# Kernel tuning notes

Measured on AMD Instinct MI355X. Metric: run time of the kernel, lower is better.

The kernel has to match this reference:

```python
import math
import jax, jax.numpy as jnp
import numpy as np

B, SX, SY, D, H = 2, 1024, 1024, 1024, 16
FULL = 1536   # padded (full_q == full_k) frame length for the two-source attention
N_CTX = 2048  # causal bias buffer size
HD = D // H
LENS_X = np.array([1024, 700])
LENS_Y = np.array([1024, 850])


def _heads(t):
    b, s, d = t.shape
    return t.reshape(b, s, H, HD).transpose(0, 2, 1, 3)  # [B,H,S,HD]


def _merge(t):
    b, h, s, hd = t.shape
    return t.transpose(0, 2, 1, 3).reshape(b, s, h * hd)


def setup_inputs() -> dict:
    key = jax.random.key(0)
    ks = jax.random.split(key, 8)
    s = 0.02
    # ragged pack/unpack index lists: take = positions in the FULL frame, fill = positions in the shrunk frame
    x_take_b = np.concatenate([np.full(l, b, np.int32) for b, l in enumerate(LENS_X)])
    x_take_p = np.concatenate([(FULL - l + np.arange(l)).astype(np.int32) for l in LENS_X])  # right-aligned
    x_fill_b = x_take_b.copy()
    x_fill_p = np.concatenate([np.arange(l, dtype=np.int32) for l in LENS_X])
    y_take_b = np.concatenate([np.full(l, b, np.int32) for b, l in enumerate(LENS_Y)])
    y_take_p = np.concatenate([np.arange(l, dtype=np.int32) for l in LENS_Y])  # left-aligned
    y_fill_b = y_take_b.copy()
    y_fill_p = y_take_p.copy()
    # additive padding mask for the self-attention over shrunk x
    mask = np.full((B, 1, 1, SX), -10000.0, np.float32)
    for b, l in enumerate(LENS_X):
        mask[b, :, :, :l] = 0.0
    return {
        "x": jax.random.normal(ks[0], (B, SX, D), jnp.float32),
        "y": jax.random.normal(ks[1], (B, SY, D), jnp.float32),
        "attention_mask_x": jnp.asarray(mask),
        "W_attn": jax.random.normal(ks[2], (D, 3 * D), jnp.float32) * s,
        "b_attn": jnp.zeros((3 * D,), jnp.float32),
        "W_2a": jax.random.normal(ks[3], (D, D), jnp.float32) * s,
        "b_2a": jnp.zeros((D,), jnp.float32),
        "W_2b": jax.random.normal(ks[4], (D, 2 * D), jnp.float32) * s,
        "b_2b": jnp.zeros((2 * D,), jnp.float32),
        "W_proj": jax.random.normal(ks[5], (2 * D, D), jnp.float32) * s,
        "b_proj": jnp.zeros((D,), jnp.float32),
        "x_take_b": jnp.asarray(x_take_b), "x_take_p": jnp.asarray(x_take_p),
        "x_fill_b": jnp.asarray(x_fill_b), "x_fill_p": jnp.asarray(x_fill_p),
        "y_take_b": jnp.asarray(y_take_b), "y_take_p": jnp.asarray(y_take_p),
        "y_fill_b": jnp.asarray(y_fill_b), "y_fill_p": jnp.asarray(y_fill_p),
    }


def reference(x, y, attention_mask_x, W_attn, b_attn, W_2a, b_2a, W_2b, b_2b,
              W_proj, b_proj, x_take_b, x_take_p, x_fill_b, x_fill_p,
              y_take_b, y_take_p, y_fill_b, y_fill_p):
    causal = jnp.tril(jnp.ones((N_CTX, N_CTX), jnp.float32))
    inv_sqrt = 1.0 / math.sqrt(HD)

    # --- branch 1: causal self-attention on shrunk x ---
    qkv = x @ W_attn + b_attn
    q, k, v = jnp.split(qkv, 3, axis=2)
    q, k, v = _heads(q), _heads(k), _heads(v)
    w = jnp.einsum('bhqd,bhkd->bhqk', q, k) * inv_sqrt  # [B,H,SX,SX]
    b1 = causal[:SX, :SX]
    w = w * b1 - 10000.0 * (1.0 - b1) + attention_mask_x
    a = jnp.einsum('bhqk,bhkd->bhqd', jax.nn.softmax(w, axis=-1), v)
    a = _merge(a)  # [B,SX,D]

    # --- branch 2: two-source attention with ragged expand/shrink ---
    q2 = _heads(x @ W_2a + b_2a)                      # [B,H,SX,HD]
    k2, v2 = jnp.split(y @ W_2b + b_2b, 2, axis=2)
    k2, v2 = _heads(k2), _heads(v2)                   # [B,H,SY,HD]
    w2 = jnp.einsum('bhqd,bhkd->bhqk', q2, k2)        # [B,H,SX,SY] (unscaled yet)
    # expand key dim: shrunk SY -> FULL
    temp = jnp.zeros((B, H, SX, FULL), w2.dtype)
    temp = temp.at[y_take_b, :, :, y_take_p].set(w2[y_fill_b, :, :, y_fill_p])
    # expand query dim: shrunk SX -> FULL
    new_w = jnp.zeros((B, H, FULL, FULL), w2.dtype)
    new_w = new_w.at[x_take_b, :, x_take_p, :].set(temp[x_fill_b, :, x_fill_p, :])
    new_v = jnp.zeros((B, H, FULL, HD), v2.dtype)
    new_v = new_v.at[y_take_b, :, y_take_p, :].set(v2[y_fill_b, :, y_fill_p, :])
    kmask = jnp.full((B, 1, 1, FULL), -10000.0, w2.dtype)
    kmask = kmask.at[y_take_b, :, :, y_take_p].set(0.0)
    new_w = new_w * inv_sqrt
    b2 = causal[:FULL, :FULL]  # ns-nd == 0 since full_q == full_k
    new_w = new_w * b2 - 10000.0 * (1.0 - b2) + kmask
    a2 = jnp.einsum('bhqk,bhkd->bhqd', jax.nn.softmax(new_w, axis=-1), new_v)  # [B,H,FULL,HD]
    # shrink query dim back: FULL -> SX
    a2s = jnp.zeros((B, H, SX, HD), a2.dtype)
    a2s = a2s.at[x_fill_b, :, x_fill_p, :].set(a2[x_take_b, :, x_take_p, :])
    a2m = _merge(a2s)  # [B,SX,D]

    out = jnp.concatenate([a, a2m], axis=2) @ W_proj + b_proj  # [B,SX,D]
    return out
```

## Files before the change

kernel.cpp:

```cpp
#include <hip/hip_runtime.h>
#include <hip/hip_bf16.h>

typedef __bf16 bf16;
typedef __attribute__((ext_vector_type(4))) __bf16 bf16x4;
typedef __attribute__((ext_vector_type(8))) __bf16 bf16x8;
typedef __attribute__((ext_vector_type(4))) float floatx4;

__device__ __forceinline__ void gl_lds16(const bf16* g, bf16* l) {
  __builtin_amdgcn_global_load_lds(
      (const __attribute__((address_space(1))) void*)g,
      (__attribute__((address_space(3))) void*)l, 16, 0, 0);
}

__global__ __launch_bounds__(256) void sentinel_kernel(float* out, int n, float code) {
  int i = blockIdx.x * 256 + threadIdx.x;
  if (i < n) out[i] = code;
}

struct TP { const float* W; bf16* WT; int K; int N; int bxn; int bid0; };

__global__ __launch_bounds__(256) void prep_kernel(TP t0, TP t1, TP t2, TP t3,
                                                   const float* __restrict__ x,
                                                   const float* __restrict__ y,
                                                   bf16* __restrict__ xb,
                                                   bf16* __restrict__ yb) {
  int bid = blockIdx.x;
  int tid = threadIdx.x;
  if (bid < 2048) {
    __shared__ float tile[64][65];
    TP t = t0;
    if (bid >= t3.bid0) t = t3;
    else if (bid >= t2.bid0) t = t2;
    else if (bid >= t1.bid0) t = t1;
    int rb = bid - t.bid0;
    int n0 = (rb % t.bxn) * 64, k0 = (rb / t.bxn) * 64;
    int tx = tid & 15, ty = tid >> 4;
#pragma unroll
    for (int i = 0; i < 4; ++i) {
      floatx4 v = *(const floatx4*)(t.W + (size_t)(k0 + ty + 16 * i) * t.N + n0 + tx * 4);
#pragma unroll
      for (int j = 0; j < 4; ++j) tile[ty + 16 * i][tx * 4 + j] = v[j];
    }
    __syncthreads();
#pragma unroll
    for (int i = 0; i < 4; ++i) {
      int nr = ty + 16 * i;
      bf16x4 o;
#pragma unroll
      for (int j = 0; j < 4; ++j) o[j] = (bf16)tile[tx * 4 + j][nr];
      *(bf16x4*)(t.WT + (size_t)(n0 + nr) * t.K + k0 + tx * 4) = o;
    }
  } else {
    long base = (long)(bid - 2048) * 4096 + (long)tid * 16;
    const float* src = x; bf16* dst = xb; long idx = base;
    if (base >= 2097152) { src = y; dst = yb; idx = base - 2097152; }
    floatx4 v0 = *(const floatx4*)(src + idx);
    floatx4 v1 = *(const floatx4*)(src + idx + 4);
    floatx4 v2 = *(const floatx4*)(src + idx + 8);
    floatx4 v3 = *(const floatx4*)(src + idx + 12);
    bf16x8 o0, o1;
#pragma unroll
    for (int i = 0; i < 4; ++i) {
      o0[i] = (bf16)v0[i]; o0[4 + i] = (bf16)v1[i];
      o1[i] = (bf16)v2[i]; o1[4 + i] = (bf16)v3[i];
    }
    *(bf16x8*)(dst + idx) = o0;
    *(bf16x8*)(dst + idx + 8) = o1;
  }
}

struct GP { const bf16* A; const bf16* WT; const float* bias; bf16* C; bf16* VT;
            int N; int ldc; int vcol0; int bxn; int bid0; };

__global__ __launch_bounds__(256) void proj3_kernel(GP g0, GP g1, GP g2) {
  __shared__ __attribute__((aligned(16))) bf16 As[128 * 64];
  __shared__ __attribute__((aligned(16))) bf16 Bs[128 * 64];
  int bid = blockIdx.x;
  GP g = g0;
  if (bid >= g2.bid0) g = g2;
  else if (bid >= g1.bid0) g = g1;
  int rb = bid - g.bid0;
  int row0 = (rb / g.bxn) * 128, col0 = (rb % g.bxn) * 128;
  const int K = 1024;
  int tid = threadIdx.x;
  int lane = tid & 63, wave = tid >> 6;
  int quad = lane >> 4, l16 = lane & 15;
  int wm = wave >> 1, wn = wave & 1;
  floatx4 acc[4][4] = {};
  for (int k0 = 0; k0 < K; k0 += 64) {
#pragma unroll
    for (int s = 0; s < 4; ++s) {
      int sl = s * 256 + tid;
      int r = sl >> 3, o = sl & 7;
      int c = (o ^ (r & 7)) * 8;
      gl_lds16(g.WT + (size_t)(col0 + r) * K + k0 + c, Bs + (size_t)sl * 8);
      gl_lds16(g.A + (size_t)(row0 + r) * K + k0 + c, As + (size_t)sl * 8);
    }
    __syncthreads();
#pragma unroll
    for (int kk = 0; kk < 2; ++kk) {
      int ko = kk * 4 + quad;
      bf16x8 afr[4], bfr[4];
#pragma unroll
      for (int r = 0; r < 4; ++r) {
        int m = wm * 64 + r * 16 + l16;
        afr[r] = *(const bf16x8*)(As + (size_t)(m * 8 + (ko ^ (m & 7))) * 8);
      }
#pragma unroll
      for (int c = 0; c < 4; ++c) {
        int n = wn * 64 + c * 16 + l16;
        bfr[c] = *(const bf16x8*)(Bs + (size_t)(n * 8 + (ko ^ (n & 7))) * 8);
      }
#pragma unroll
      for (int r = 0; r < 4; ++r)
#pragma unroll
        for (int c = 0; c < 4; ++c)
          acc[r][c] = __builtin_amdgcn_mfma_f32_16x16x32_bf16(afr[r], bfr[c], acc[r][c], 0, 0, 0);
    }
    __syncthreads();
  }
  int inV = (col0 >= g.vcol0);
#pragma unroll
  for (int c = 0; c < 4; ++c) {
    int gcol = col0 + wn * 64 + c * 16 + l16;
    float bv = g.bias[gcol];
    if (inV) {
      int vcol = gcol - g.vcol0;
      int hh = vcol >> 6, dd = vcol & 63;
#pragma unroll
      for (int r = 0; r < 4; ++r) {
        int row = row0 + wm * 64 + r * 16 + quad * 4;
        int bb = row >> 10, key = row & 1023;
        bf16x4 pk;
#pragma unroll
        for (int e = 0; e < 4; ++e) pk[e] = (bf16)(acc[r][c][e] + bv);
        *(bf16x4*)(g.VT + ((size_t)((bb << 4) + hh)) * 65536 + (size_t)dd * 1024 + key) = pk;
      }
    } else {
#pragma unroll
      for (int r = 0; r < 4; ++r) {
        int grow = row0 + wm * 64 + r * 16 + quad * 4;
#pragma unroll
        for (int e = 0; e < 4; ++e)
          g.C[(size_t)(grow + e) * g.ldc + gcol] = (bf16)(acc[r][c][e] + bv);
      }
    }
  }
}

__global__ __launch_bounds__(256) void gemm_out_kernel(const bf16* __restrict__ A,
                                                       const bf16* __restrict__ WT,
                                                       const float* __restrict__ bias,
                                                       float* __restrict__ C,
                                                       int N, int K) {
  __shared__ __attribute__((aligned(16))) bf16 As[64 * 64];
  __shared__ __attribute__((aligned(16))) bf16 Bs[64 * 64];
  int tid = threadIdx.x;
  int lane = tid & 63, wave = tid >> 6;
  int quad = lane >> 4, l16 = lane & 15;
  int row0 = blockIdx.y * 64, col0 = blockIdx.x * 64;
  floatx4 acc[4] = {};
  for (int k0 = 0; k0 < K; k0 += 64) {
#pragma unroll
    for (int s = 0; s < 2; ++s) {
      int sl = s * 256 + tid;
      int r = sl >> 3, o = sl & 7;
      int c = (o ^ (r & 7)) * 8;
      gl_lds16(A + (size_t)(row0 + r) * K + k0 + c, As + (size_t)sl * 8);
      gl_lds16(WT + (size_t)(col0 + r) * K + k0 + c, Bs + (size_t)sl * 8);
    }
    __syncthreads();
#pragma unroll
    for (int kk = 0; kk < 2; ++kk) {
      int ko = kk * 4 + quad;
      int m = wave * 16 + l16;
      bf16x8 af = *(const bf16x8*)(As + (size_t)(m * 8 + (ko ^ (m & 7))) * 8);
#pragma unroll
      for (int nt = 0; nt < 4; ++nt) {
        int n = nt * 16 + l16;
        bf16x8 bf = *(const bf16x8*)(Bs + (size_t)(n * 8 + (ko ^ (n & 7))) * 8);
        acc[nt] = __builtin_amdgcn_mfma_f32_16x16x32_bf16(af, bf, acc[nt], 0, 0, 0);
      }
    }
    __syncthreads();
  }
#pragma unroll
  for (int nt = 0; nt < 4; ++nt) {
    int gcol = col0 + nt * 16 + l16;
    float bv = bias[gcol];
#pragma unroll
    for (int e = 0; e < 4; ++e) {
      int grow = row0 + wave * 16 + quad * 4 + e;
      C[(size_t)grow * N + gcol] = acc[nt][e] + bv;
    }
  }
}

struct AP {
  const bf16* Q; const bf16* K; const bf16* VT; bf16* O;
  int qstride, kstride, ostride;
  long qbatch, kbatch, obatch;
  int coff0, coff1, klen0, klen1, qv0, qv1;
};

__global__ __launch_bounds__(512) void attn2x_kernel(AP a0, AP a1, float scale) {
  __shared__ __attribute__((aligned(16))) bf16 Ks[2][64 * 64];
  __shared__ __attribute__((aligned(16))) bf16 Vs[2][64 * 64];
  __shared__ __attribute__((aligned(16))) bf16 Ps[8][16 * 72];
  AP a = (blockIdx.x >> 8) ? a1 : a0;
  int tid = threadIdx.x;
  int lane = tid & 63, w = tid >> 6;
  int quad = lane >> 4, l16 = lane & 15;
  int r = blockIdx.x & 255;
  int b = r >> 7, h = (r >> 3) & 15, qt = r & 7;
  int coff = b ? a.coff1 : a.coff0;
  int klen = b ? a.klen1 : a.klen0;
  int qv = b ? a.qv1 : a.qv0;
  int qbase = qt * 128;
  int wq0 = qbase + w * 16;
  int qi = wq0 + l16;
  const bf16* Q   = a.Q + (size_t)b * a.qbatch + h * 64;
  const bf16* Kp  = a.K + (size_t)b * a.kbatch + h * 64;
  const bf16* VTp = a.VT + (size_t)(b * 16 + h) * 65536;
  bf16* O = a.O + (size_t)b * a.obatch + h * 64;

  bf16x8 aq0 = *(const bf16x8*)(Q + (size_t)qi * a.qstride + quad * 8);
  bf16x8 aq1 = *(const bf16x8*)(Q + (size_t)qi * a.qstride + 32 + quad * 8);

  floatx4 o[4] = {};
  float part = 0.f;

  int kend = klen < qbase + 128 + coff ? klen : qbase + 128 + coff;
  int nblk = (kend + 63) >> 6;
  int wkend0 = wq0 + 16 + coff;
  int wkend = klen < wkend0 ? klen : wkend0;

  const float KSC = scale * 1.44269504f;
  const float KOFF = -5.77078016f;

  auto stage = [&](int buf, int j0) {
    int row = tid >> 3, ch = tid & 7;
    gl_lds16(Kp + (size_t)(j0 + row) * a.kstride + ((ch ^ (row & 7)) * 8),
             Ks[buf] + (size_t)tid * 8);
    gl_lds16(VTp + (size_t)row * 1024 + j0 + ((ch ^ (row & 7)) * 8),
             Vs[buf] + (size_t)tid * 8);
  };

  stage(0, 0);
  for (int t = 0; t < nblk; ++t) {
    int j0 = t * 64;
    __syncthreads();
    if (t + 1 < nblk) stage((t + 1) & 1, j0 + 64);
    if (j0 >= wkend) continue;
    const bf16* Kt = Ks[t & 1];
    const bf16* Vt = Vs[t & 1];

    floatx4 sv[4];
#pragma unroll
    for (int nt = 0; nt < 4; ++nt) {
      int key = nt * 16 + l16;
      int sl0 = key * 8 + (quad ^ (key & 7));
      int sl1 = key * 8 + ((quad + 4) ^ (key & 7));
      bf16x8 bk0 = *(const bf16x8*)(Kt + (size_t)sl0 * 8);
      bf16x8 bk1 = *(const bf16x8*)(Kt + (size_t)sl1 * 8);
      floatx4 z = {};
      z = __builtin_amdgcn_mfma_f32_16x16x32_bf16(bk0, aq0, z, 0, 0, 0);
      z = __builtin_amdgcn_mfma_f32_16x16x32_bf16(bk1, aq1, z, 0, 0, 0);
      sv[nt] = z;
    }
    bool fullv = (j0 + 63 <= wq0 + coff) && (j0 + 63 < klen);
#pragma unroll
    for (int nt = 0; nt < 4; ++nt) {
      bf16x4 pk;
#pragma unroll
      for (int e = 0; e < 4; ++e) {
        float arg = fmaf(sv[nt][e], KSC, KOFF);
        if (!fullv) {
          int j = j0 + nt * 16 + quad * 4 + e;
          arg = (j <= qi + coff && j < klen) ? arg : -60.0f;
        }
        float p = exp2f(arg);
        part += p;
        pk[e] = (bf16)p;
      }
      *(bf16x4*)(Ps[w] + l16 * 72 + nt * 16 + quad * 4) = pk;
    }
    bf16x8 pb0 = *(const bf16x8*)(Ps[w] + l16 * 72 + quad * 8);
    bf16x8 pb1 = *(const bf16x8*)(Ps[w] + l16 * 72 + 32 + quad * 8);
#pragma unroll
    for (int ct = 0; ct < 4; ++ct) {
      int dd = ct * 16 + l16;
      int sl0 = dd * 8 + (quad ^ (dd & 7));
      int sl1 = dd * 8 + ((quad + 4) ^ (dd & 7));
      bf16x8 va0 = *(const bf16x8*)(Vt + (size_t)sl0 * 8);
      bf16x8 va1 = *(const bf16x8*)(Vt + (size_t)sl1 * 8);
      o[ct] = __builtin_amdgcn_mfma_f32_16x16x32_bf16(va0, pb0, o[ct], 0, 0, 0);
      o[ct] = __builtin_amdgcn_mfma_f32_16x16x32_bf16(va1, pb1, o[ct], 0, 0, 0);
    }
  }
  part += __shfl_xor(part, 16);
  part += __shfl_xor(part, 32);
  float rinv = 1.0f / part;
#pragma unroll
  for (int ct = 0; ct < 4; ++ct) {
    bf16x4 pk;
#pragma unroll
    for (int e = 0; e < 4; ++e) {
      float val = o[ct][e] * rinv;
      if (qi >= qv) val = 0.f;
      pk[e] = (bf16)val;
    }
    *(bf16x4*)(O + (size_t)qi * a.ostride + ct * 16 + quad * 4) = pk;
  }
}

extern "C" void kernel_launch(void* const* d_in, const int* in_sizes, int n_in,
                              void* d_out, int out_size, void* d_ws, size_t ws_size,
                              hipStream_t stream) {
  const float* x      = (const float*)d_in[0];
  const float* y      = (const float*)d_in[1];
  const float* W_attn = (const float*)d_in[3];
  const float* b_attn = (const float*)d_in[4];
  const float* W_2a   = (const float*)d_in[5];
  const float* b_2a   = (const float*)d_in[6];
  const float* W_2b   = (const float*)d_in[7];
  const float* b_2b   = (const float*)d_in[8];
  const float* W_proj = (const float*)d_in[9];
  const float* b_proj = (const float*)d_in[10];
  bf16* ws = (bf16*)d_ws;
  float* out = (float*)d_out;

  const int LX0 = 1024, LX1 = 700, LY0 = 1024, LY1 = 850;
  const float scale = 0.125f;
  const size_t WS_FAST = (size_t)25165824 * 2;

  if (ws_size < WS_FAST) {
    sentinel_kernel<<<(out_size + 255) / 256, 256, 0, stream>>>(
        out, out_size, (float)(ws_size >> 20) + 10.0f);
    return;
  }

  bf16* qk1  = ws;
  bf16* q2   = ws + (size_t) 4194304;
  bf16* k2   = ws + (size_t) 6291456;
  bf16* VT1  = ws + (size_t) 8388608;
  bf16* VT2  = ws + (size_t)10485760;
  bf16* xb   = ws + (size_t)12582912;
  bf16* yb   = ws + (size_t)14680064;
  bf16* cat  = ws + (size_t)12582912;
  bf16* WaT  = ws + (size_t)16777216;
  bf16* W2aT = ws + (size_t)19922944;
  bf16* W2bT = ws + (size_t)20971520;
  bf16* WpT  = ws + (size_t)23068672;

  TP t0 = {W_attn, WaT, 1024, 3072, 48, 0};
  TP t1 = {W_2a, W2aT, 1024, 1024, 16, 768};
  TP t2 = {W_2b, W2bT, 1024, 2048, 32, 1024};
  TP t3 = {W_proj, WpT, 2048, 1024, 16, 1536};
  prep_kernel<<<3072, 256, 0, stream>>>(t0, t1, t2, t3, x, y, xb, yb);

  GP g0 = {xb, WaT, b_attn, qk1, VT1, 3072, 2048, 2048, 24, 0};
  GP g1 = {xb, W2aT, b_2a, q2, nullptr, 1024, 1024, 1 << 30, 8, 384};
  GP g2 = {yb, W2bT, b_2b, k2, VT2, 2048, 1024, 1024, 16, 512};
  proj3_kernel<<<768, 256, 0, stream>>>(g0, g1, g2);

  AP a0 = {qk1, qk1 + 1024, VT1, cat, 2048, 2048, 2048,
           (long)1024 * 2048, (long)1024 * 2048, (long)1024 * 2048,
           0, 0, LX0, LX1, 1024, 1024};
  AP a1 = {q2, k2, VT2, cat + 1024, 1024, 1024, 2048,
           (long)1024 * 1024, (long)1024 * 1024, (long)1024 * 2048,
           1536 - LX0, 1536 - LX1, LY0, LY1, LX0, LX1};
  attn2x_kernel<<<512, 512, 0, stream>>>(a0, a1, scale);

  gemm_out_kernel<<<dim3(16, 32), 256, 0, stream>>>(cat, WpT, b_proj, out, 1024, 2048);
}
```

Measured before the change: 233.8 us.

## Rework projection GEMM as 256x256 tile double-buffered ping-pong pipeline

Moves the fused QKV/q2/kv2 projection GEMM to 256x256 output tiles with 512 threads per block. LDS is double-buffered and each K-step is split into four phases, so global-to-LDS loads for the next tiles overlap the current MFMA work, with barriers and s_setprio steering the wave schedule. The goal is more operand reuse and hiding load latency instead of a full sync per K-step. The trade-off is that the grid shrinks from 768 to 192 blocks, fewer than the CU count, and the 128 KB LDS per block limits occupancy.

```diff
diff --git a/kernel.cpp b/kernel.cpp
--- a/kernel.cpp
+++ b/kernel.cpp
@@ -72,53 +72,161 @@
 struct GP { const bf16* A; const bf16* WT; const float* bias; bf16* C; bf16* VT;
             int N; int ldc; int vcol0; int bxn; int bid0; };
 
-__global__ __launch_bounds__(256) void proj3_kernel(GP g0, GP g1, GP g2) {
-  __shared__ __attribute__((aligned(16))) bf16 As[128 * 64];
-  __shared__ __attribute__((aligned(16))) bf16 Bs[128 * 64];
+__global__ __launch_bounds__(512, 2) void proj3_kernel(GP g0, GP g1, GP g2) {
+  __shared__ __attribute__((aligned(16))) bf16 As[2][16384];
+  __shared__ __attribute__((aligned(16))) bf16 Bs[2][16384];
   int bid = blockIdx.x;
   GP g = g0;
   if (bid >= g2.bid0) g = g2;
   else if (bid >= g1.bid0) g = g1;
   int rb = bid - g.bid0;
-  int row0 = (rb / g.bxn) * 128, col0 = (rb % g.bxn) * 128;
-  const int K = 1024;
+  int row0 = (rb / g.bxn) * 256, col0 = (rb % g.bxn) * 256;
   int tid = threadIdx.x;
   int lane = tid & 63, wave = tid >> 6;
   int quad = lane >> 4, l16 = lane & 15;
-  int wm = wave >> 1, wn = wave & 1;
-  floatx4 acc[4][4] = {};
-  for (int k0 = 0; k0 < K; k0 += 64) {
-#pragma unroll
-    for (int s = 0; s < 4; ++s) {
-      int sl = s * 256 + tid;
-      int r = sl >> 3, o = sl & 7;
-      int c = (o ^ (r & 7)) * 8;
-      gl_lds16(g.WT + (size_t)(col0 + r) * K + k0 + c, Bs + (size_t)sl * 8);
-      gl_lds16(g.A + (size_t)(row0 + r) * K + k0 + c, As + (size_t)sl * 8);
-    }
-    __syncthreads();
+  int wm = wave >> 2, wn = wave & 3;
+  const bf16* Ag = g.A + (size_t)row0 * 1024;
+  const bf16* Bg = g.WT + (size_t)col0 * 1024;
+
+  auto stA = [&](bf16* L, int k0, int qr) {
+#pragma unroll
+    for (int t = 0; t < 2; ++t) {
+      int i = t * 512 + tid;
+      int rh = i >> 3, o = i & 7;
+      int m = qr * 64 + (rh & 63) + ((rh & 64) << 1);
+      gl_lds16(Ag + (size_t)m * 1024 + k0 + ((o ^ (m & 7)) * 8),
+               L + (size_t)(m * 8 + o) * 8);
+    }
+  };
+  auto stB = [&](bf16* L, int k0, int qc) {
+#pragma unroll
+    for (int t = 0; t < 2; ++t) {
+      int i = t * 512 + tid;
+      int rh = i >> 3, o = i & 7;
+      int n = qc * 32 + (rh & 31) + ((rh >> 5) << 6);
+      gl_lds16(Bg + (size_t)n * 1024 + k0 + ((o ^ (n & 7)) * 8),
+               L + (size_t)(n * 8 + o) * 8);
+    }
+  };
+
+  floatx4 acc[8][4] = {};
+
+  stA(As[0], 0, 0); stB(Bs[0], 0, 0);
+  stA(As[0], 0, 1); stB(Bs[0], 0, 1);
+  stB(Bs[1], 64, 0);
+  stA(As[1], 64, 1);
+  asm volatile("s_waitcnt vmcnt(4)" ::: "memory");
+  __builtin_amdgcn_s_barrier();
+
+#pragma unroll 2
+  for (int T = 0; T < 16; ++T) {
+    int cb = T & 1, nb = cb ^ 1;
+    const bf16* Ac = As[cb];
+    const bf16* Bc = Bs[cb];
+    bf16x8 fA[2][4], fB[2][2], fA2[2][4], fB2[2][2];
+
 #pragma unroll
     for (int kk = 0; kk < 2; ++kk) {
       int ko = kk * 4 + quad;
-      bf16x8 afr[4], bfr[4];
 #pragma unroll
       for (int r = 0; r < 4; ++r) {
-        int m = wm * 64 + r * 16 + l16;
-        afr[r] = *(const bf16x8*)(As + (size_t)(m * 8 + (ko ^ (m & 7))) * 8);
-      }
-#pragma unroll
-      for (int c = 0; c < 4; ++c) {
+        int m = wm * 128 + r * 16 + l16;
+        fA[kk][r] = *(const bf16x8*)(Ac + (size_t)(m * 8 + (ko ^ (m & 7))) * 8);
+      }
+#pragma unroll
+      for (int c = 0; c < 2; ++c) {
         int n = wn * 64 + c * 16 + l16;
-        bfr[c] = *(const bf16x8*)(Bs + (size_t)(n * 8 + (ko ^ (n & 7))) * 8);
-      }
+        fB[kk][c] = *(const bf16x8*)(Bc + (size_t)(n * 8 + (ko ^ (n & 7))) * 8);
+      }
+    }
+    stA(As[nb], (T + 1) * 64, 0);
+    asm volatile("s_waitcnt lgkmcnt(0)" ::: "memory");
+    __builtin_amdgcn_s_barrier();
+    __builtin_amdgcn_sched_barrier(0);
+    __builtin_amdgcn_s_setprio(1);
+#pragma unroll
+    for (int kk = 0; kk < 2; ++kk)
 #pragma unroll
       for (int r = 0; r < 4; ++r)
 #pragma unroll
-        for (int c = 0; c < 4; ++c)
-          acc[r][c] = __builtin_amdgcn_mfma_f32_16x16x32_bf16(afr[r], bfr[c], acc[r][c], 0, 0, 0);
-    }
-    __syncthreads();
-  }
+        for (int c = 0; c < 2; ++c)
+          acc[r][c] = __builtin_amdgcn_mfma_f32_16x16x32_bf16(fA[kk][r], fB[kk][c], acc[r][c], 0, 0, 0);
+    __builtin_amdgcn_s_setprio(0);
+    __builtin_amdgcn_s_barrier();
+
+#pragma unroll
+    for (int kk = 0; kk < 2; ++kk) {
+      int ko = kk * 4 + quad;
+#pragma unroll
+      for (int r = 0; r < 4; ++r) {
+        int m = wm * 128 + 64 + r * 16 + l16;
+        fA2[kk][r] = *(const bf16x8*)(Ac + (size_t)(m * 8 + (ko ^ (m & 7))) * 8);
+      }
+    }
+    stB(Bs[nb], (T + 1) * 64, 1);
+    asm volatile("s_waitcnt lgkmcnt(0)" ::: "memory");
+    __builtin_amdgcn_s_barrier();
+    __builtin_amdgcn_sched_barrier(0);
+    __builtin_amdgcn_s_setprio(1);
+#pragma unroll
+    for (int kk = 0; kk < 2; ++kk)
+#pragma unroll
+      for (int r = 0; r < 4; ++r)
+#pragma unroll
+        for (int c = 0; c < 2; ++c)
+          acc[4 + r][c] = __builtin_amdgcn_mfma_f32_16x16x32_bf16(fA2[kk][r], fB[kk][c], acc[4 + r][c], 0, 0, 0);
+    __builtin_amdgcn_s_setprio(0);
+    __builtin_amdgcn_s_barrier();
+
+#pragma unroll
+    for (int kk = 0; kk < 2; ++kk) {
+      int ko = kk * 4 + quad;
+#pragma unroll
+      for (int c = 0; c < 2; ++c) {
+        int n = wn * 64 + 32 + c * 16 + l16;
+        fB2[kk][c] = *(const bf16x8*)(Bc + (size_t)(n * 8 + (ko ^ (n & 7))) * 8);
+      }
+    }
+    stB(Bs[cb], (T + 2) * 64, 0);
+    asm volatile("s_waitcnt lgkmcnt(0)" ::: "memory");
+    __builtin_amdgcn_s_barrier();
+    __builtin_amdgcn_sched_barrier(0);
+    __builtin_amdgcn_s_setprio(1);
+#pragma unroll
+    for (int kk = 0; kk < 2; ++kk)
+#pragma unroll
+      for (int r = 0; r < 4; ++r)
+#pragma unroll
+        for (int c = 0; c < 2; ++c)
+          acc[4 + r][2 + c] = __builtin_amdgcn_mfma_f32_16x16x32_bf16(fA2[kk][r], fB2[kk][c], acc[4 + r][2 + c], 0, 0, 0);
+    __builtin_amdgcn_s_setprio(0);
+    __builtin_amdgcn_s_barrier();
+
+#pragma unroll
+    for (int kk = 0; kk < 2; ++kk) {
+      int ko = kk * 4 + quad;
+#pragma unroll
+      for (int r = 0; r < 4; ++r) {
+        int m = wm * 128 + r * 16 + l16;
+        fA[kk][r] = *(const bf16x8*)(Ac + (size_t)(m * 8 + (ko ^ (m & 7))) * 8);
+      }
+    }
+    stA(As[cb], (T + 2) * 64, 1);
+    asm volatile("s_waitcnt vmcnt(4) lgkmcnt(0)" ::: "memory");
+    __builtin_amdgcn_s_barrier();
+    __builtin_amdgcn_sched_barrier(0);
+    __builtin_amdgcn_s_setprio(1);
+#pragma unroll
+    for (int kk = 0; kk < 2; ++kk)
+#pragma unroll
+      for (int r = 0; r < 4; ++r)
+#pragma unroll
+        for (int c = 0; c < 2; ++c)
+          acc[r][2 + c] = __builtin_amdgcn_mfma_f32_16x16x32_bf16(fA[kk][r], fB2[kk][c], acc[r][2 + c], 0, 0, 0);
+    __builtin_amdgcn_s_setprio(0);
+    __builtin_amdgcn_s_barrier();
+  }
+
   int inV = (col0 >= g.vcol0);
 #pragma unroll
   for (int c = 0; c < 4; ++c) {
@@ -128,8 +236,8 @@
       int vcol = gcol - g.vcol0;
       int hh = vcol >> 6, dd = vcol & 63;
 #pragma unroll
-      for (int r = 0; r < 4; ++r) {
-        int row = row0 + wm * 64 + r * 16 + quad * 4;
+      for (int r = 0; r < 8; ++r) {
+        int row = row0 + wm * 128 + r * 16 + quad * 4;
         int bb = row >> 10, key = row & 1023;
         bf16x4 pk;
 #pragma unroll
@@ -138,8 +246,8 @@
       }
     } else {
 #pragma unroll
-      for (int r = 0; r < 4; ++r) {
-        int grow = row0 + wm * 64 + r * 16 + quad * 4;
+      for (int r = 0; r < 8; ++r) {
+        int grow = row0 + wm * 128 + r * 16 + quad * 4;
 #pragma unroll
         for (int e = 0; e < 4; ++e)
           g.C[(size_t)(grow + e) * g.ldc + gcol] = (bf16)(acc[r][c][e] + bv);
@@ -359,10 +467,10 @@
   TP t3 = {W_proj, WpT, 2048, 1024, 16, 1536};
   prep_kernel<<<3072, 256, 0, stream>>>(t0, t1, t2, t3, x, y, xb, yb);
 
-  GP g0 = {xb, WaT, b_attn, qk1, VT1, 3072, 2048, 2048, 24, 0};
-  GP g1 = {xb, W2aT, b_2a, q2, nullptr, 1024, 1024, 1 << 30, 8, 384};
-  GP g2 = {yb, W2bT, b_2b, k2, VT2, 2048, 1024, 1024, 16, 512};
-  proj3_kernel<<<768, 256, 0, stream>>>(g0, g1, g2);
+  GP g0 = {xb, WaT, b_attn, qk1, VT1, 3072, 2048, 2048, 12, 0};
+  GP g1 = {xb, W2aT, b_2a, q2, nullptr, 1024, 1024, 1 << 30, 4, 96};
+  GP g2 = {yb, W2bT, b_2b, k2, VT2, 2048, 1024, 1024, 8, 128};
+  proj3_kernel<<<192, 512, 0, stream>>>(g0, g1, g2);
 
   AP a0 = {qk1, qk1 + 1024, VT1, cat, 2048, 2048, 2048,
            (long)1024 * 2048, (long)1024 * 2048, (long)1024 * 2048,
```

Measured after the change: 234.2 us. Within noise of the previous version (+0.2%).
